# Performance work log

Measured on AMD Instinct MI355X. Metric: run time of the kernel, lower is better.

The kernel has to match this reference:

```python
import jax, jax.numpy as jnp
import numpy as np
jax.config.update("jax_enable_x64", True)

HASH_PRIMES = [2654435761, 2246822519, 3266489917, 2028178513, 1220703125, 1610612741,
               805306457, 402653189, 3674653429, 2860486313, 1073676287, 2971215073,
               1500450271, 3267000013, 2654435789, 4049292737]
SCALE_WINDOWS = [1, 2, 4, 8]

VOCAB = 1024
BUCKETS = 4_000_000
NUM_SCALES = 4
E = 4                 # embed_per_scale
BOUNDARY = 2          # condition_boundary (min(2, num_scales))
SIGN_BITS = 8
BATCH, T = 32, 2048


def _hash_scale(tokens, scale_idx):
    # rolling shift-xor-mul hash over a small fixed window (<=8)
    window = SCALE_WINDOWS[scale_idx]
    primes = HASH_PRIMES[:window]
    h = jnp.zeros_like(tokens)
    Tlen = tokens.shape[1]
    for i in range(window):
        off = i + 1
        if off >= Tlen:
            continue
        shifted = jnp.pad(tokens[:, :-off], ((0, 0), (off, 0)))  # zeros at front
        h = h ^ (shifted * primes[i])
    return h % BUCKETS


def setup_inputs() -> dict:
    key = jax.random.key(0)
    ks = jax.random.split(key, 6)
    tokens = jax.random.randint(ks[0], (BATCH, T), 0, VOCAB, dtype=jnp.int64)
    tables = [0.02 * jax.random.normal(ks[1 + s], (BUCKETS, E), dtype=jnp.float32)
              for s in range(NUM_SCALES)]
    # nn.Linear(short_dim=BOUNDARY*E, SIGN_BITS, bias=False): weight [out, in]
    short_dim = BOUNDARY * E
    bound = 1.0 / np.sqrt(short_dim)
    cond_w = jax.random.uniform(ks[5], (SIGN_BITS, short_dim),
                                minval=-bound, maxval=bound, dtype=jnp.float32)
    return {"tokens": tokens, "table0": tables[0], "table1": tables[1],
            "table2": tables[2], "table3": tables[3], "cond_w": cond_w}


def reference(tokens, table0, table1, table2, table3, cond_w):
    tables = [table0, table1, table2, table3]
    keys = [_hash_scale(tokens, s) for s in range(NUM_SCALES)]
    # short scales: plain hashed gather
    short_embeds = [tables[s][keys[s]] for s in range(BOUNDARY)]  # [B,T,E] each
    # condition long scales on short-scale sign bits
    short_cat = jnp.concatenate(short_embeds, axis=-1)            # [B,T,BOUNDARY*E]
    cond_logits = jnp.einsum('btd,od->bto', short_cat, cond_w)    # [B,T,SIGN_BITS]
    sign_bits = (cond_logits > 0).astype(jnp.int64)
    cond_key = jnp.zeros(tokens.shape, dtype=jnp.int64)
    for i in range(SIGN_BITS):
        cond_key = cond_key ^ (sign_bits[:, :, i] * HASH_PRIMES[i])
    long_embeds = []
    for s in range(BOUNDARY, NUM_SCALES):
        k = (keys[s] ^ cond_key) % BUCKETS
        long_embeds.append(tables[s][k])
    return jnp.concatenate(short_embeds + long_embeds, axis=-1)   # [B,T,NUM_SCALES*E]
```

## Files before the change

kernel.cpp:

```cpp
#include <hip/hip_runtime.h>
#include <cstdint>


constexpr int TT = 2048;
constexpr int BB = 32;
constexpr uint32_t BUCKETS = 4000000u;
constexpr int ELEMS_PER_BLOCK = 64;

__device__ constexpr uint64_t PRIMES64[8] = {
    2654435761ull, 2246822519ull, 3266489917ull, 2028178513ull,
    1220703125ull, 1610612741ull,  805306457ull,  402653189ull};

extern "C" __global__ void __launch_bounds__(256)
pyramid_kernel(const int* __restrict__ tokens,
               const float* __restrict__ t0,
               const float* __restrict__ t1,
               const float* __restrict__ t2,
               const float* __restrict__ t3,
               const float* __restrict__ cw,
               float* __restrict__ out)
{
    __shared__ int   stok[ELEMS_PER_BLOCK + 8];
    __shared__ float scw[64];

    const int tid = threadIdx.x;
    const int el  = tid >> 2;
    const int r   = tid & 3;

    const int blocksPerRow = TT / ELEMS_PER_BLOCK;
    const int b     = blockIdx.x / blocksPerRow;
    const int tBase = (blockIdx.x % blocksPerRow) * ELEMS_PER_BLOCK;
    const int* row  = tokens + (size_t)b * TT;

    if (tid < ELEMS_PER_BLOCK + 8) {
        const int t = tBase - 8 + tid;
        stok[tid] = (t >= 0) ? row[t] : 0;
    }
    if (tid < 64) scw[tid] = cw[tid];
    __syncthreads();

    uint64_t x = 0;
    x ^= (uint64_t)(uint32_t)stok[el + 7] * PRIMES64[0];
    const uint32_t k0 = (uint32_t)(x % BUCKETS);
    x ^= (uint64_t)(uint32_t)stok[el + 6] * PRIMES64[1];
    const uint32_t k1 = (uint32_t)(x % BUCKETS);
    x ^= (uint64_t)(uint32_t)stok[el + 5] * PRIMES64[2];
    x ^= (uint64_t)(uint32_t)stok[el + 4] * PRIMES64[3];
    const uint32_t k2h = (uint32_t)(x % BUCKETS);
    x ^= (uint64_t)(uint32_t)stok[el + 3] * PRIMES64[4];
    x ^= (uint64_t)(uint32_t)stok[el + 2] * PRIMES64[5];
    x ^= (uint64_t)(uint32_t)stok[el + 1] * PRIMES64[6];
    x ^= (uint64_t)(uint32_t)stok[el + 0] * PRIMES64[7];
    const uint32_t k3h = (uint32_t)(x % BUCKETS);

    const float*  sp = (r & 1) ? t1 : t0;
    const uint32_t sk = (r & 1) ? k1 : k0;
    const float4 v1 = *(const float4*)(sp + (size_t)sk * 4);

    const int wl   = threadIdx.x & 63;
    const int base = wl & ~3;
    float cat[8];
    cat[0] = __shfl(v1.x, base + 0, 64);
    cat[1] = __shfl(v1.y, base + 0, 64);
    cat[2] = __shfl(v1.z, base + 0, 64);
    cat[3] = __shfl(v1.w, base + 0, 64);
    cat[4] = __shfl(v1.x, base + 1, 64);
    cat[5] = __shfl(v1.y, base + 1, 64);
    cat[6] = __shfl(v1.z, base + 1, 64);
    cat[7] = __shfl(v1.w, base + 1, 64);

    uint32_t ck = 0;
#pragma unroll
    for (int o = 0; o < 8; ++o) {
        float acc = 0.f;
#pragma unroll
        for (int d = 0; d < 8; ++d) acc = fmaf(cat[d], scw[o * 8 + d], acc);
        if (acc > 0.f) ck ^= (uint32_t)PRIMES64[o];
    }

    const uint32_t kk2 = (k2h ^ ck) % BUCKETS;
    const uint32_t kk3 = (k3h ^ ck) % BUCKETS;
    const float*   lp  = (r & 1) ? t3 : t2;
    const uint32_t lk  = (r & 1) ? kk3 : kk2;
    const float4 v2 = *(const float4*)(lp + (size_t)lk * 4);

    const float4 vo = (r < 2) ? v1 : v2;
    const int elemG = b * TT + tBase + el;
    *(float4*)(out + (size_t)elemG * 16 + r * 4) = vo;
}

extern "C" void kernel_launch(void* const* d_in, const int* in_sizes, int n_in,
                              void* d_out, int out_size, void* d_ws, size_t ws_size,
                              hipStream_t stream)
{
    const int*   tokens = (const int*)d_in[0];
    const float* t0     = (const float*)d_in[1];
    const float* t1     = (const float*)d_in[2];
    const float* t2     = (const float*)d_in[3];
    const float* t3     = (const float*)d_in[4];
    const float* cw     = (const float*)d_in[5];
    float*       out    = (float*)d_out;

    const dim3 grid(BB * (TT / ELEMS_PER_BLOCK));
    pyramid_kernel<<<grid, 256, 0, stream>>>(tokens, t0, t1, t2, t3, cw, out);
}
```

Measured before the change: 185.9 us.

## Assign one thread per token with all four gathers, drop cross-lane shuffles

Each thread now handles one whole token instead of four threads sharing it. It computes all hashes, issues both short-scale gathers back to back, and builds the condition vector from its own registers instead of cross-lane shuffles. It then writes all 64 output bytes itself. Blocks shrink to 64 threads, so total threads drop fourfold. The intent is to remove redundant hash/matmul work and shuffles, at the cost of fewer loads in flight per SM unless occupancy compensates and less coalesced stores.

```diff
diff --git a/kernel.cpp b/kernel.cpp
--- a/kernel.cpp
+++ b/kernel.cpp
@@ -5,13 +5,13 @@
 constexpr int TT = 2048;
 constexpr int BB = 32;
 constexpr uint32_t BUCKETS = 4000000u;
-constexpr int ELEMS_PER_BLOCK = 64;
+constexpr int EPB = 64;
 
 __device__ constexpr uint64_t PRIMES64[8] = {
     2654435761ull, 2246822519ull, 3266489917ull, 2028178513ull,
     1220703125ull, 1610612741ull,  805306457ull,  402653189ull};
 
-extern "C" __global__ void __launch_bounds__(256)
+extern "C" __global__ void __launch_bounds__(64)
 pyramid_kernel(const int* __restrict__ tokens,
                const float* __restrict__ t0,
                const float* __restrict__ t1,
@@ -20,30 +20,33 @@
                const float* __restrict__ cw,
                float* __restrict__ out)
 {
-    __shared__ int   stok[ELEMS_PER_BLOCK + 8];
+    __shared__ int   stok[EPB + 8];
     __shared__ float scw[64];
 
     const int tid = threadIdx.x;
-    const int el  = tid >> 2;
-    const int r   = tid & 3;
-
-    const int blocksPerRow = TT / ELEMS_PER_BLOCK;
+    const int blocksPerRow = TT / EPB;
     const int b     = blockIdx.x / blocksPerRow;
-    const int tBase = (blockIdx.x % blocksPerRow) * ELEMS_PER_BLOCK;
+    const int tBase = (blockIdx.x % blocksPerRow) * EPB;
     const int* row  = tokens + (size_t)b * TT;
 
-    if (tid < ELEMS_PER_BLOCK + 8) {
+    {
         const int t = tBase - 8 + tid;
         stok[tid] = (t >= 0) ? row[t] : 0;
+        if (tid < 8) stok[64 + tid] = row[tBase + 56 + tid];
     }
-    if (tid < 64) scw[tid] = cw[tid];
+    scw[tid] = cw[tid];
     __syncthreads();
 
-    uint64_t x = 0;
-    x ^= (uint64_t)(uint32_t)stok[el + 7] * PRIMES64[0];
+    const int el = tid;
+
+    uint64_t x = (uint64_t)(uint32_t)stok[el + 7] * PRIMES64[0];
     const uint32_t k0 = (uint32_t)(x % BUCKETS);
     x ^= (uint64_t)(uint32_t)stok[el + 6] * PRIMES64[1];
     const uint32_t k1 = (uint32_t)(x % BUCKETS);
+
+    const float4 v0 = ((const float4* __restrict__)t0)[k0];
+    const float4 v1 = ((const float4* __restrict__)t1)[k1];
+
     x ^= (uint64_t)(uint32_t)stok[el + 5] * PRIMES64[2];
     x ^= (uint64_t)(uint32_t)stok[el + 4] * PRIMES64[3];
     const uint32_t k2h = (uint32_t)(x % BUCKETS);
@@ -53,22 +56,7 @@
     x ^= (uint64_t)(uint32_t)stok[el + 0] * PRIMES64[7];
     const uint32_t k3h = (uint32_t)(x % BUCKETS);
 
-    const float*  sp = (r & 1) ? t1 : t0;
-    const uint32_t sk = (r & 1) ? k1 : k0;
-    const float4 v1 = *(const float4*)(sp + (size_t)sk * 4);
-
-    const int wl   = threadIdx.x & 63;
-    const int base = wl & ~3;
-    float cat[8];
-    cat[0] = __shfl(v1.x, base + 0, 64);
-    cat[1] = __shfl(v1.y, base + 0, 64);
-    cat[2] = __shfl(v1.z, base + 0, 64);
-    cat[3] = __shfl(v1.w, base + 0, 64);
-    cat[4] = __shfl(v1.x, base + 1, 64);
-    cat[5] = __shfl(v1.y, base + 1, 64);
-    cat[6] = __shfl(v1.z, base + 1, 64);
-    cat[7] = __shfl(v1.w, base + 1, 64);
-
+    const float cat[8] = {v0.x, v0.y, v0.z, v0.w, v1.x, v1.y, v1.z, v1.w};
     uint32_t ck = 0;
 #pragma unroll
     for (int o = 0; o < 8; ++o) {
@@ -80,13 +68,15 @@
 
     const uint32_t kk2 = (k2h ^ ck) % BUCKETS;
     const uint32_t kk3 = (k3h ^ ck) % BUCKETS;
-    const float*   lp  = (r & 1) ? t3 : t2;
-    const uint32_t lk  = (r & 1) ? kk3 : kk2;
-    const float4 v2 = *(const float4*)(lp + (size_t)lk * 4);
+    const float4 v2 = ((const float4* __restrict__)t2)[kk2];
+    const float4 v3 = ((const float4* __restrict__)t3)[kk3];
 
-    const float4 vo = (r < 2) ? v1 : v2;
-    const int elemG = b * TT + tBase + el;
-    *(float4*)(out + (size_t)elemG * 16 + r * 4) = vo;
+    float4* __restrict__ o16 =
+        (float4*)(out + ((size_t)blockIdx.x * EPB + el) * 16);
+    o16[0] = v0;
+    o16[1] = v1;
+    o16[2] = v2;
+    o16[3] = v3;
 }
 
 extern "C" void kernel_launch(void* const* d_in, const int* in_sizes, int n_in,
@@ -101,6 +91,6 @@
     const float* cw     = (const float*)d_in[5];
     float*       out    = (float*)d_out;
 
-    const dim3 grid(BB * (TT / ELEMS_PER_BLOCK));
-    pyramid_kernel<<<grid, 256, 0, stream>>>(tokens, t0, t1, t2, t3, cw, out);
+    const dim3 grid(BB * (TT / EPB));
+    pyramid_kernel<<<grid, EPB, 0, stream>>>(tokens, t0, t1, t2, t3, cw, out);
 }
```

New measurement: 187.5 us. About the same (+0.9%).
